# Kernel tuning notes

Hardware: AMD Instinct MI355X
Metric: run time of the kernel (lower is better)

The kernel has to match this reference:

```python
import jax, jax.numpy as jnp
import numpy as np
from jax import lax

HEADS = 8
DIM_HEAD = 8
SCALE = DIM_HEAD ** (-0.5)
UP = 64  # nn.Upsample(scale_factor=64), nearest


def _conv_s8(x, w, b):
    # Conv2d(inner, inner, 11x11, stride 8, padding 2) + exact GELU
    y = lax.conv_general_dilated(x, w, window_strides=(8, 8),
                                 padding=((2, 2), (2, 2)),
                                 dimension_numbers=('NCHW', 'OIHW', 'NCHW'))
    return jax.nn.gelu(y + b[None, :, None, None], approximate=False)


def setup_inputs() -> dict:
    key = jax.random.key(0)
    ks = jax.random.split(key, 8)
    b, c, h, w = 2, 64, 48, 48
    inner = HEADS * DIM_HEAD  # 64
    f = jax.random.normal(ks[0], (b, c, h, w), jnp.float32)
    w_qkv = jax.random.normal(ks[1], (inner * 3, c, 1, 1), jnp.float32) * 0.05
    wq = jax.random.normal(ks[2], (inner, inner, 11, 11), jnp.float32) * 0.02
    bq = jax.random.normal(ks[3], (inner,), jnp.float32) * 0.02
    wk = jax.random.normal(ks[4], (inner, inner, 11, 11), jnp.float32) * 0.02
    bk = jax.random.normal(ks[5], (inner,), jnp.float32) * 0.02
    pos_h = jax.random.normal(ks[6], (DIM_HEAD, h), jnp.float32) * SCALE
    pos_w = jax.random.normal(ks[7], (DIM_HEAD, w), jnp.float32) * SCALE
    return {"f": f, "w_qkv": w_qkv, "wq": wq, "bq": bq, "wk": wk,
            "bk": bk, "pos_h": pos_h, "pos_w": pos_w}


def reference(f, w_qkv, wq, bq, wk, bk, pos_h, pos_w):
    b, c, h, w = f.shape
    inner = HEADS * DIM_HEAD
    # 1x1 conv to qkv
    qkv = jnp.einsum('oc,bchw->bohw', w_qkv[:, :, 0, 0], f)
    q, k, v = jnp.split(qkv, 3, axis=1)  # each [b, inner, h, w]
    # positional logits from pre-conv q
    q_full = q.reshape(b, HEADS, DIM_HEAD, h * w)
    emb = (pos_h[:, :, None] + pos_w[:, None, :]).reshape(DIM_HEAD, h * w)
    pos_logits = jnp.einsum('bhci,cj->bhij', q_full, emb)  # [b,H,hw,hw]
    # strided conv + gelu on q,k
    qd = _conv_s8(q, wq, bq)
    kd = _conv_s8(k, wk, bk)
    m = qd.shape[-1]  # downsampled side
    qd = qd.reshape(b, HEADS, DIM_HEAD, m * m) * SCALE
    kd = kd.reshape(b, HEADS, DIM_HEAD, m * m)
    vv = v.reshape(b, HEADS, DIM_HEAD, h * w)
    dots = jnp.einsum('bhci,bhcj->bhij', qd, kd)  # [b,H,m^2,m^2]
    # nearest upsample x64 on last two dims
    dots = jnp.repeat(jnp.repeat(dots, UP, axis=-2), UP, axis=-1)
    attn = jax.nn.softmax(dots + pos_logits, axis=-1)
    fmap = jnp.einsum('bhij,bhcj->bhci', attn, vv)
    return fmap.reshape(b, inner, h, w)
```

## Files before the change

### kernel.cpp

```cpp
#include <hip/hip_runtime.h>
#include <math.h>

#define HW 2304
#define O192 192
#define SCALE_F 0.35355339059327373f

__global__ __launch_bounds__(256) void qkv_kernel(
    const float* __restrict__ F, const float* __restrict__ W,
    float* __restrict__ QKV, float* __restrict__ V2) {
  __shared__ __align__(16) float sW[384];
  int blk = blockIdx.x;
  int idx0 = blk * 256;
  int r0 = idx0 / HW;
  int r1 = (idx0 + 255) / HW;
  int tid = threadIdx.x;
  if (tid < 192) {
    int g = tid >> 6, c = tid & 63;
    sW[tid]       = W[((r0 & 63) + g * 64) * 64 + c];
    sW[192 + tid] = W[((r1 & 63) + g * 64) * 64 + c];
  }
  __syncthreads();
  int idx = idx0 + tid;
  int p  = idx % HW;
  int r  = idx / HW;
  int o0 = r & 63;
  int b  = r >> 6;
  const float4* w4 = (const float4*)(sW + ((r == r0) ? 0 : 192));
  const float* f = F + (b * 64) * HW + p;
  float aq = 0.f, ak = 0.f, av = 0.f;
  #pragma unroll 4
  for (int c4 = 0; c4 < 16; c4++) {
    float4 wq = w4[c4];
    float4 wk = w4[16 + c4];
    float4 wv = w4[32 + c4];
    float f0 = f[(c4 * 4 + 0) * HW];
    float f1 = f[(c4 * 4 + 1) * HW];
    float f2 = f[(c4 * 4 + 2) * HW];
    float f3 = f[(c4 * 4 + 3) * HW];
    aq = fmaf(wq.x, f0, aq); ak = fmaf(wk.x, f0, ak); av = fmaf(wv.x, f0, av);
    aq = fmaf(wq.y, f1, aq); ak = fmaf(wk.y, f1, ak); av = fmaf(wv.y, f1, av);
    aq = fmaf(wq.z, f2, aq); ak = fmaf(wk.z, f2, ak); av = fmaf(wv.z, f2, av);
    aq = fmaf(wq.w, f3, aq); ak = fmaf(wk.w, f3, ak); av = fmaf(wv.w, f3, av);
  }
  float* qp = QKV + (b * HW + p) * O192;
  qp[o0]      = aq;
  qp[o0 + 64] = ak;
  V2[(((b << 3) + (o0 >> 3)) * HW + p) * 8 + (o0 & 7)] = av;
}

__global__ __launch_bounds__(256) void conv_kernel(
    const float* __restrict__ QKV, const float* __restrict__ Wq,
    const float* __restrict__ Bq, const float* __restrict__ Wk,
    const float* __restrict__ Bk, float* __restrict__ QD) {
  __shared__ float sW[7744];
  __shared__ float sRed[4 * 64 * 6];
  int blk = blockIdx.x;
  int xcd = blk & 7;
  int T = xcd >> 2, b = (xcd >> 1) & 1, s = xcd & 1;
  int idx = (blk >> 3) * 2 + s;
  int o  = idx / 6;
  int oy = idx % 6;
  const float* Wg = T ? Wk : Wq;
  for (int i = threadIdx.x; i < 7744; i += 256) sW[i] = Wg[o * 7744 + i];
  __syncthreads();
  int wv = threadIdx.x >> 6;
  int c  = threadIdx.x & 63;
  const float* base = QKV + b * (HW * O192) + T * 64 + c;
  float acc[6];
  #pragma unroll
  for (int ox = 0; ox < 6; ox++) acc[ox] = 0.f;
  for (int kyi = 0; kyi < 3; kyi++) {
    int ky = wv * 3 + kyi;
    if (ky > 10) break;
    int y = oy * 8 - 2 + ky;
    if ((unsigned)y < 48u) {
      float xrow[48];
      #pragma unroll
      for (int x = 0; x < 48; x++) xrow[x] = base[(y * 48 + x) * O192];
      #pragma unroll
      for (int kx = 0; kx < 11; kx++) {
        float wt = sW[c * 121 + ky * 11 + kx];
        #pragma unroll
        for (int ox = 0; ox < 6; ox++) {
          int x = ox * 8 - 2 + kx;
          if (x >= 0 && x < 48) acc[ox] = fmaf(xrow[x], wt, acc[ox]);
        }
      }
    }
  }
  #pragma unroll
  for (int ox = 0; ox < 6; ox++) sRed[(wv * 64 + c) * 6 + ox] = acc[ox];
  __syncthreads();
  if (threadIdx.x < 64) {
    int t = threadIdx.x;
    float r[6];
    #pragma unroll
    for (int ox = 0; ox < 6; ox++)
      r[ox] = sRed[t * 6 + ox] + sRed[(64 + t) * 6 + ox]
            + sRed[(128 + t) * 6 + ox] + sRed[(192 + t) * 6 + ox];
    #pragma unroll
    for (int off = 32; off; off >>= 1) {
      #pragma unroll
      for (int ox = 0; ox < 6; ox++) r[ox] += __shfl_down(r[ox], off, 64);
    }
    if (t == 0) {
      float bias = T ? Bk[o] : Bq[o];
      #pragma unroll
      for (int ox = 0; ox < 6; ox++) {
        float g = r[ox] + bias;
        float ge = 0.5f * g * (1.0f + erff(g * 0.70710678118654752f));
        QD[((T * 2 + b) * 64 + o) * 36 + oy * 6 + ox] = ge;
      }
    }
  }
}

__global__ __launch_bounds__(256) void dots_kernel(
    const float* __restrict__ QD, float* __restrict__ E) {
  int idx = blockIdx.x * 256 + threadIdx.x;
  if (idx >= 16 * 36 * 36) return;
  int J  = idx % 36;
  int I  = (idx / 36) % 36;
  int bh = idx / 1296;
  int b = bh >> 3, h = bh & 7;
  float acc = 0.f;
  #pragma unroll
  for (int c8 = 0; c8 < 8; c8++) {
    float qv = QD[((0 + b) * 64 + h * 8 + c8) * 36 + I];
    float kv = QD[((2 + b) * 64 + h * 8 + c8) * 36 + J];
    acc = fmaf(qv, kv, acc);
  }
  E[idx] = __expf(SCALE_F * acc);
}

__global__ __launch_bounds__(512, 4) void attn_kernel(
    const float* __restrict__ QKV, const float* __restrict__ V2,
    const float* __restrict__ E, const float* __restrict__ PH,
    const float* __restrict__ PW, float* __restrict__ out) {
  __shared__ __align__(16) float sV[1152 * 8];
  __shared__ __align__(16) float sPHT[48 * 8];
  __shared__ __align__(16) float sPWT[48 * 8];
  __shared__ float sE[36];
  __shared__ float sRed[8 * 64 * 9];
  __shared__ float sZinv[64];
  int bh = blockIdx.x / 36;
  int I  = blockIdx.x % 36;
  int b = bh >> 3, h = bh & 7;
  int tid = threadIdx.x;
  if (tid < 384) sPHT[tid] = PH[(tid & 7) * 48 + (tid >> 3)];
  else { int i = tid - 384; sPWT[i] = PW[(i & 7) * 48 + (i >> 3)]; }
  if (tid < 256) { int i = tid + 128; sPWT[i] = PW[(i & 7) * 48 + (i >> 3)]; }
  if (tid < 36) sE[tid] = E[bh * 1296 + I * 36 + tid];
  int wv = tid >> 6, lane = tid & 63;
  const float* qr = QKV + (b * HW + I * 64 + lane) * O192 + h * 8;
  float4 qa = *(const float4*)qr;
  float4 qb = *(const float4*)(qr + 4);
  __syncthreads();
  float eB[48];
  #pragma unroll
  for (int x = 0; x < 48; x++) {
    float4 p0 = *(const float4*)(sPWT + x * 8);
    float4 p1 = *(const float4*)(sPWT + x * 8 + 4);
    float v = qa.x * p0.x + qa.y * p0.y + qa.z * p0.z + qa.w * p0.w
            + qb.x * p1.x + qb.y * p1.y + qb.z * p1.z + qb.w * p1.w;
    eB[x] = __expf(v);
  }
  float acc[9];
  #pragma unroll
  for (int c = 0; c < 9; c++) acc[c] = 0.f;
  const float4* vsrc = (const float4*)(V2 + (size_t)bh * (HW * 8));
  for (int p = 0; p < 2; p++) {
    __syncthreads();
    {
      float4* dst = (float4*)sV;
      #pragma unroll
      for (int k = 0; k < 5; k++) {
        int i = tid + k * 512;
        if (i < 2304) dst[i] = vsrc[p * 2304 + i];
      }
    }
    __syncthreads();
    #pragma unroll
    for (int t = 0; t < 3; t++) {
      int jy = p * 24 + wv * 3 + t;
      float4 h0 = *(const float4*)(sPHT + jy * 8);
      float4 h1 = *(const float4*)(sPHT + jy * 8 + 4);
      float eA = __expf(qa.x * h0.x + qa.y * h0.y + qa.z * h0.z + qa.w * h0.w
                      + qb.x * h1.x + qb.y * h1.y + qb.z * h1.z + qb.w * h1.w);
      #pragma unroll
      for (int c3 = 0; c3 < 6; c3++) {
        float tA = eA * sE[(jy * 6 + c3) >> 3];
        const float* vp = sV + (((jy - p * 24) * 48) + c3 * 8) * 8;
        #pragma unroll
        for (int u = 0; u < 8; u++) {
          float wgt = tA * eB[c3 * 8 + u];
          float4 lo = *(const float4*)(vp + u * 8);
          float4 hi = *(const float4*)(vp + u * 8 + 4);
          acc[0] = fmaf(wgt, lo.x, acc[0]);
          acc[1] = fmaf(wgt, lo.y, acc[1]);
          acc[2] = fmaf(wgt, lo.z, acc[2]);
          acc[3] = fmaf(wgt, lo.w, acc[3]);
          acc[4] = fmaf(wgt, hi.x, acc[4]);
          acc[5] = fmaf(wgt, hi.y, acc[5]);
          acc[6] = fmaf(wgt, hi.z, acc[6]);
          acc[7] = fmaf(wgt, hi.w, acc[7]);
          acc[8] += wgt;
        }
      }
    }
  }
  {
    float* rp = sRed + (wv * 64 + lane) * 9;
    #pragma unroll
    for (int c = 0; c < 9; c++) rp[c] = acc[c];
  }
  __syncthreads();
  if (tid < 64) {
    float z = 0.f;
    #pragma unroll
    for (int w = 0; w < 8; w++) z += sRed[(w * 64 + tid) * 9 + 8];
    sZinv[tid] = 1.0f / z;
  }
  __syncthreads();
  {
    int c = tid >> 6, r = tid & 63;
    float v = 0.f;
    #pragma unroll
    for (int w = 0; w < 8; w++) v += sRed[(w * 64 + r) * 9 + c];
    out[(b * 64 + h * 8 + c) * HW + I * 64 + r] = v * sZinv[r];
  }
}

extern "C" void kernel_launch(void* const* d_in, const int* in_sizes, int n_in,
                              void* d_out, int out_size, void* d_ws, size_t ws_size,
                              hipStream_t stream) {
  const float* F    = (const float*)d_in[0];
  const float* Wqkv = (const float*)d_in[1];
  const float* Wq   = (const float*)d_in[2];
  const float* Bq   = (const float*)d_in[3];
  const float* Wk   = (const float*)d_in[4];
  const float* Bk   = (const float*)d_in[5];
  const float* PH   = (const float*)d_in[6];
  const float* PW   = (const float*)d_in[7];
  float* out = (float*)d_out;

  float* ws  = (float*)d_ws;
  float* QKV = ws;
  float* V2  = QKV + 2 * HW * O192;
  float* QD  = V2 + 2 * 8 * HW * 8;
  float* E   = QD + 2 * 2 * 64 * 36;

  qkv_kernel <<<1152, 256, 0, stream>>>(F, Wqkv, QKV, V2);
  conv_kernel<<<1536, 256, 0, stream>>>(QKV, Wq, Bq, Wk, Bk, QD);
  dots_kernel<<<81,   256, 0, stream>>>(QD, E);
  attn_kernel<<<576,  512, 0, stream>>>(QKV, V2, E, PH, PW, out);
}
```

Before: 143.4 us.

## Split attention over key quarters with register-blocked queries and combine pass

The attention kernel now processes 256 query rows per block against a quarter of the key positions. Each thread holds 4 queries in registers so every V value read from shared memory is reused four times. The V slice is loaded with direct global-to-LDS DMA, and the exp(pos_h) terms are precomputed into shared memory. Partial numerators and normalisers are written to workspace, and a new combine kernel sums them and divides. This adds an extra launch and extra global traffic in exchange for fewer LDS reads per FMA.

```diff
diff --git a/kernel.cpp b/kernel.cpp
--- a/kernel.cpp
+++ b/kernel.cpp
@@ -4,6 +4,13 @@
 #define HW 2304
 #define O192 192
 #define SCALE_F 0.35355339059327373f
+
+typedef unsigned int u32;
+typedef __attribute__((address_space(1))) const u32 gu32;
+typedef __attribute__((address_space(3))) u32 lu32;
+__device__ __forceinline__ void dma16(const void* g, void* l) {
+  __builtin_amdgcn_global_load_lds((gu32*)g, (lu32*)l, 16, 0, 0);
+}
 
 __global__ __launch_bounds__(256) void qkv_kernel(
     const float* __restrict__ F, const float* __restrict__ W,
@@ -133,102 +140,143 @@
   E[idx] = __expf(SCALE_F * acc);
 }
 
+#define OFF_V   0
+#define OFF_EA  4608
+#define OFF_PHT 7680
+#define OFF_PWT 8064
+#define OFF_E4  8448
+#define OFF_U   8592
+#define SBUF_N  13200
+
 __global__ __launch_bounds__(512, 4) void attn_kernel(
     const float* __restrict__ QKV, const float* __restrict__ V2,
     const float* __restrict__ E, const float* __restrict__ PH,
-    const float* __restrict__ PW, float* __restrict__ out) {
-  __shared__ __align__(16) float sV[1152 * 8];
-  __shared__ __align__(16) float sPHT[48 * 8];
-  __shared__ __align__(16) float sPWT[48 * 8];
-  __shared__ float sE[36];
-  __shared__ float sRed[8 * 64 * 9];
-  __shared__ float sZinv[64];
-  int bh = blockIdx.x / 36;
-  int I  = blockIdx.x % 36;
+    const float* __restrict__ PW, float* __restrict__ Pnum,
+    float* __restrict__ PZ) {
+  __shared__ __align__(16) float sB[SBUF_N];
+  int blk = blockIdx.x;
+  int bh = blk / 36;
+  int rem = blk - bh * 36;
+  int q = rem & 3, S = rem >> 2;
   int b = bh >> 3, h = bh & 7;
   int tid = threadIdx.x;
-  if (tid < 384) sPHT[tid] = PH[(tid & 7) * 48 + (tid >> 3)];
-  else { int i = tid - 384; sPWT[i] = PW[(i & 7) * 48 + (i >> 3)]; }
-  if (tid < 256) { int i = tid + 128; sPWT[i] = PW[(i & 7) * 48 + (i >> 3)]; }
-  if (tid < 36) sE[tid] = E[bh * 1296 + I * 36 + tid];
-  int wv = tid >> 6, lane = tid & 63;
-  const float* qr = QKV + (b * HW + I * 64 + lane) * O192 + h * 8;
-  float4 qa = *(const float4*)qr;
-  float4 qb = *(const float4*)(qr + 4);
-  __syncthreads();
-  float eB[48];
-  #pragma unroll
-  for (int x = 0; x < 48; x++) {
-    float4 p0 = *(const float4*)(sPWT + x * 8);
-    float4 p1 = *(const float4*)(sPWT + x * 8 + 4);
-    float v = qa.x * p0.x + qa.y * p0.y + qa.z * p0.z + qa.w * p0.w
-            + qb.x * p1.x + qb.y * p1.y + qb.z * p1.z + qb.w * p1.w;
-    eB[x] = __expf(v);
-  }
-  float acc[9];
-  #pragma unroll
-  for (int c = 0; c < 9; c++) acc[c] = 0.f;
-  const float4* vsrc = (const float4*)(V2 + (size_t)bh * (HW * 8));
-  for (int p = 0; p < 2; p++) {
+  int w = tid >> 6, lane = tid & 63;
+  if (tid < 384) {
+    sB[OFF_PHT + tid] = PH[(tid & 7) * 48 + (tid >> 3)];
+    sB[OFF_PWT + tid] = PW[(tid & 7) * 48 + (tid >> 3)];
+  }
+  if (tid < 144) {
+    int J = tid >> 2, k = tid & 3;
+    sB[OFF_E4 + tid] = E[bh * 1296 + (S * 4 + k) * 36 + J];
+  }
+  {
+    int row = tid >> 1, half = tid & 1;
+    *(float4*)(sB + OFF_U + tid * 4) =
+      *(const float4*)(QKV + (b * HW + S * 256 + row) * O192 + h * 8 + half * 4);
+  }
+  {
+    const char* src = (const char*)(V2 + (size_t)bh * (HW * 8) + q * 4608);
+    for (int m = w; m < 18; m += 8)
+      dma16(src + m * 1024 + lane * 16, (char*)(sB + OFF_V) + m * 1024);
+  }
+  __syncthreads();
+  #pragma unroll
+  for (int m = 0; m < 6; m++) {
+    int flat = tid + m * 512;
+    int jyL = flat >> 8, rl = flat & 255;
+    int ln = rl >> 2, kk = rl & 3;
+    const float* qp = sB + OFF_U + (kk * 64 + ln) * 8;
+    const float* pp = sB + OFF_PHT + (q * 12 + jyL) * 8;
+    float d = qp[0]*pp[0]+qp[1]*pp[1]+qp[2]*pp[2]+qp[3]*pp[3]
+            + qp[4]*pp[4]+qp[5]*pp[5]+qp[6]*pp[6]+qp[7]*pp[7];
+    sB[OFF_EA + flat] = __expf(d);
+  }
+  float eB[4][6];
+  #pragma unroll
+  for (int k = 0; k < 4; k++) {
+    const float* qp = sB + OFF_U + (k * 64 + lane) * 8;
+    #pragma unroll
+    for (int i = 0; i < 6; i++) {
+      const float* pp = sB + OFF_PWT + (w * 6 + i) * 8;
+      float d = qp[0]*pp[0]+qp[1]*pp[1]+qp[2]*pp[2]+qp[3]*pp[3]
+              + qp[4]*pp[4]+qp[5]*pp[5]+qp[6]*pp[6]+qp[7]*pp[7];
+      eB[k][i] = __expf(d);
+    }
+  }
+  __syncthreads();
+  float acc[4][9];
+  #pragma unroll
+  for (int k = 0; k < 4; k++)
+    #pragma unroll
+    for (int c = 0; c < 9; c++) acc[k][c] = 0.f;
+  const float4* sV4 = (const float4*)(sB + OFF_V);
+  for (int jyL = 0; jyL < 12; jyL++) {
+    float4 eAk = *(const float4*)(sB + OFF_EA + jyL * 256 + lane * 4);
+    int cb = (q * 12 + jyL) * 48 + w * 6;
+    int J0 = cb >> 6, J1 = (cb + 5) >> 6;
+    int ib = 64 - (cb & 63);
+    float4 e0 = *(const float4*)(sB + OFF_E4 + J0 * 4);
+    float4 e1 = *(const float4*)(sB + OFF_E4 + J1 * 4);
+    float a0[4] = {eAk.x*e0.x, eAk.y*e0.y, eAk.z*e0.z, eAk.w*e0.w};
+    float a1[4] = {eAk.x*e1.x, eAk.y*e1.y, eAk.z*e1.z, eAk.w*e1.w};
+    #pragma unroll
+    for (int i = 0; i < 6; i++) {
+      float4 vlo = sV4[(jyL * 48 + w * 6 + i) * 2];
+      float4 vhi = sV4[(jyL * 48 + w * 6 + i) * 2 + 1];
+      bool sel = (i < ib);
+      #pragma unroll
+      for (int k = 0; k < 4; k++) {
+        float wgt = (sel ? a0[k] : a1[k]) * eB[k][i];
+        acc[k][0] = fmaf(wgt, vlo.x, acc[k][0]);
+        acc[k][1] = fmaf(wgt, vlo.y, acc[k][1]);
+        acc[k][2] = fmaf(wgt, vlo.z, acc[k][2]);
+        acc[k][3] = fmaf(wgt, vlo.w, acc[k][3]);
+        acc[k][4] = fmaf(wgt, vhi.x, acc[k][4]);
+        acc[k][5] = fmaf(wgt, vhi.y, acc[k][5]);
+        acc[k][6] = fmaf(wgt, vhi.z, acc[k][6]);
+        acc[k][7] = fmaf(wgt, vhi.w, acc[k][7]);
+        acc[k][8] += wgt;
+      }
+    }
+  }
+  float* sU = sB + OFF_U;
+  #pragma unroll
+  for (int k = 0; k < 4; k++) {
+    #pragma unroll
+    for (int c = 0; c < 9; c++) sU[(w * 64 + lane) * 9 + c] = acc[k][c];
     __syncthreads();
     {
-      float4* dst = (float4*)sV;
-      #pragma unroll
-      for (int k = 0; k < 5; k++) {
-        int i = tid + k * 512;
-        if (i < 2304) dst[i] = vsrc[p * 2304 + i];
+      int c = tid >> 6, r = tid & 63;
+      float num = 0.f;
+      #pragma unroll
+      for (int ww = 0; ww < 8; ww++) num += sU[(ww * 64 + r) * 9 + c];
+      Pnum[((q * 16 + bh) * 8 + c) * HW + S * 256 + k * 64 + r] = num;
+      if (tid < 64) {
+        float z = 0.f;
+        #pragma unroll
+        for (int ww = 0; ww < 8; ww++) z += sU[(ww * 64 + tid) * 9 + 8];
+        PZ[(q * 16 + bh) * HW + S * 256 + k * 64 + tid] = z;
       }
     }
     __syncthreads();
-    #pragma unroll
-    for (int t = 0; t < 3; t++) {
-      int jy = p * 24 + wv * 3 + t;
-      float4 h0 = *(const float4*)(sPHT + jy * 8);
-      float4 h1 = *(const float4*)(sPHT + jy * 8 + 4);
-      float eA = __expf(qa.x * h0.x + qa.y * h0.y + qa.z * h0.z + qa.w * h0.w
-                      + qb.x * h1.x + qb.y * h1.y + qb.z * h1.z + qb.w * h1.w);
-      #pragma unroll
-      for (int c3 = 0; c3 < 6; c3++) {
-        float tA = eA * sE[(jy * 6 + c3) >> 3];
-        const float* vp = sV + (((jy - p * 24) * 48) + c3 * 8) * 8;
-        #pragma unroll
-        for (int u = 0; u < 8; u++) {
-          float wgt = tA * eB[c3 * 8 + u];
-          float4 lo = *(const float4*)(vp + u * 8);
-          float4 hi = *(const float4*)(vp + u * 8 + 4);
-          acc[0] = fmaf(wgt, lo.x, acc[0]);
-          acc[1] = fmaf(wgt, lo.y, acc[1]);
-          acc[2] = fmaf(wgt, lo.z, acc[2]);
-          acc[3] = fmaf(wgt, lo.w, acc[3]);
-          acc[4] = fmaf(wgt, hi.x, acc[4]);
-          acc[5] = fmaf(wgt, hi.y, acc[5]);
-          acc[6] = fmaf(wgt, hi.z, acc[6]);
-          acc[7] = fmaf(wgt, hi.w, acc[7]);
-          acc[8] += wgt;
-        }
-      }
-    }
-  }
-  {
-    float* rp = sRed + (wv * 64 + lane) * 9;
-    #pragma unroll
-    for (int c = 0; c < 9; c++) rp[c] = acc[c];
-  }
-  __syncthreads();
-  if (tid < 64) {
-    float z = 0.f;
-    #pragma unroll
-    for (int w = 0; w < 8; w++) z += sRed[(w * 64 + tid) * 9 + 8];
-    sZinv[tid] = 1.0f / z;
-  }
-  __syncthreads();
-  {
-    int c = tid >> 6, r = tid & 63;
-    float v = 0.f;
-    #pragma unroll
-    for (int w = 0; w < 8; w++) v += sRed[(w * 64 + r) * 9 + c];
-    out[(b * 64 + h * 8 + c) * HW + I * 64 + r] = v * sZinv[r];
-  }
+  }
+}
+
+__global__ __launch_bounds__(256) void combine_kernel(
+    const float* __restrict__ Pnum, const float* __restrict__ PZ,
+    float* __restrict__ out) {
+  int t = blockIdx.x * 256 + threadIdx.x;
+  int row = t % HW;
+  int rc = t / HW;
+  int c = rc & 7, bh = rc >> 3;
+  float num = 0.f, z = 0.f;
+  #pragma unroll
+  for (int q = 0; q < 4; q++) {
+    num += Pnum[((q * 16 + bh) * 8 + c) * HW + row];
+    z   += PZ[(q * 16 + bh) * HW + row];
+  }
+  int b = bh >> 3, h = bh & 7;
+  out[(b * 64 + h * 8 + c) * HW + row] = num / z;
 }
 
 extern "C" void kernel_launch(void* const* d_in, const int* in_sizes, int n_in,
@@ -244,14 +292,17 @@
   const float* PW   = (const float*)d_in[7];
   float* out = (float*)d_out;
 
-  float* ws  = (float*)d_ws;
-  float* QKV = ws;
-  float* V2  = QKV + 2 * HW * O192;
-  float* QD  = V2 + 2 * 8 * HW * 8;
-  float* E   = QD + 2 * 2 * 64 * 36;
-
-  qkv_kernel <<<1152, 256, 0, stream>>>(F, Wqkv, QKV, V2);
-  conv_kernel<<<1536, 256, 0, stream>>>(QKV, Wq, Bq, Wk, Bk, QD);
-  dots_kernel<<<81,   256, 0, stream>>>(QD, E);
-  attn_kernel<<<576,  512, 0, stream>>>(QKV, V2, E, PH, PW, out);
-}
+  float* ws   = (float*)d_ws;
+  float* QKV  = ws;
+  float* V2   = QKV + 2 * HW * O192;
+  float* QD   = V2 + 2 * 8 * HW * 8;
+  float* E    = QD + 2 * 2 * 64 * 36;
+  float* Pnum = E + 16 * 36 * 36;
+  float* PZ   = Pnum + 4 * 16 * 8 * HW;
+
+  qkv_kernel    <<<1152, 256, 0, stream>>>(F, Wqkv, QKV, V2);
+  conv_kernel   <<<1536, 256, 0, stream>>>(QKV, Wq, Bq, Wk, Bk, QD);
+  dots_kernel   <<<81,   256, 0, stream>>>(QD, E);
+  attn_kernel   <<<576,  512, 0, stream>>>(QKV, V2, E, PH, PW, Pnum, PZ);
+  combine_kernel<<<1152, 256, 0, stream>>>(Pnum, PZ, out);
+}
```

Result: no change. 141.8 us (-1.1%).
